# Optimization experiments

Hardware: AMD Instinct MI355X
Metric: run time of the kernel (lower is better)

## Reference

```python
import jax, jax.numpy as jnp
import numpy as np

B, L, K, D = 1024, 128, 16, 512
NUM_FEATURES, NUM_LABELS, NUM_NEG = 100000, 131072, 2048
EPS = 0.1
C = 2.0 + EPS  # spherical kernel constant


def safe_log(x, eps=1e-08):
    return jnp.log(jnp.maximum(x, eps))


def safe_normalize(x, axis=-1, eps=0.0001):
    norm = jnp.linalg.norm(x, axis=axis, keepdims=True)
    return x / jnp.maximum(norm, eps)


def setup_inputs() -> dict:
    key = jax.random.key(0)
    k0, k1, k2, k3, k4 = jax.random.split(key, 5)
    indices = jax.random.randint(k0, (B, L), 0, NUM_FEATURES)
    mask = jnp.ones((B, L), jnp.float32)
    labels = jax.random.randint(k1, (B, K), 0, NUM_LABELS)
    label_mask = jnp.ones((B, K), jnp.float32)
    neg_indices = jax.random.randint(k2, (NUM_NEG,), 0, NUM_LABELS)
    embed_table = jax.random.normal(k3, (NUM_FEATURES, D), jnp.float32) * 0.02
    W_kernel = jax.random.normal(k4, (D, NUM_LABELS), jnp.float32) * 0.02  # nnx.Linear kernel (in, out)
    return {"indices": indices, "mask": mask, "labels": labels,
            "label_mask": label_mask, "neg_indices": neg_indices,
            "embed_table": embed_table, "W_kernel": W_kernel}


def reference(indices, mask, labels, label_mask, neg_indices, embed_table, W_kernel):
    # MeanEmbedding encoder
    embeds = embed_table[indices]                                  # [B, L, D]
    sum_embeds = jnp.sum(embeds * mask[:, :, None], axis=1)        # [B, D]
    enc = sum_embeds / jnp.maximum(jnp.sum(mask, axis=1, keepdims=True), 1.0)
    query = safe_normalize(enc, axis=-1)                           # [B, D]
    W = safe_normalize(W_kernel.T, axis=-1)                        # [NUM_LABELS, D]

    safe_labels = jnp.maximum(labels, 0)
    all_indices = jnp.concatenate([safe_labels.reshape(-1), neg_indices])  # [B*K + NN]
    W_subset = W[all_indices]                                      # [B*K+NN, D]

    # spherical Yat kernel: dot^2 / max(C - 2*dot, eps)
    dot = jnp.clip(query @ W_subset.T, -0.999, 0.999)              # [B, B*K+NN]
    scores = dot ** 2 / jnp.maximum(C - 2.0 * dot, EPS)

    idx_offsets = jnp.arange(B)[:, None] * K + jnp.arange(K)[None, :]
    pos_scores = jnp.take_along_axis(scores, idx_offsets, axis=1)  # [B, K]
    neg_scores = scores[:, B * K:]                                 # [B, NN]
    all_scores = jnp.concatenate([pos_scores, neg_scores], axis=1) + 1e-08
    log_Z = jax.scipy.special.logsumexp(safe_log(all_scores), axis=1)
    log_probs = safe_log(pos_scores + 1e-08) - log_Z[:, None]
    return -jnp.sum(log_probs * label_mask) / (jnp.sum(label_mask) + 1e-06)
```

## Files before the change

kernel.cpp:

```cpp
#include <hip/hip_runtime.h>
#include <hip/hip_bf16.h>

#define BDIM 1024
#define LDIM 128
#define KDIM 16
#define DDIM 512
#define NLAB 131072
#define NNEG 2048
#define NPOS (BDIM * KDIM)
#define NSUB (NPOS + NNEG)
#define EPSV 0.1f
#define CV 2.1f
#define NBUCK 512
#define GT_BLOCKS (NBUCK * 8)

typedef __attribute__((ext_vector_type(8))) short s8v;
typedef __attribute__((ext_vector_type(4))) float f4v;
typedef __attribute__((ext_vector_type(4))) float fv4;

static __device__ __forceinline__ unsigned short f2bf(float x) {
    union { float f; unsigned u; } v; v.f = x;
    unsigned r = v.u + 0x7FFF + ((v.u >> 16) & 1);
    return (unsigned short)(r >> 16);
}
static __device__ __forceinline__ float bf2f(unsigned short h) {
    return __uint_as_float((unsigned)h << 16);
}

__global__ __launch_bounds__(256) void init_kernel(float* __restrict__ norms2,
                                                   float* __restrict__ Zrow,
                                                   float* __restrict__ accum,
                                                   int* __restrict__ ticket) {
    int j = blockIdx.x * 256 + threadIdx.x;
    if (j < NSUB) norms2[j] = 0.f;
    if (j < BDIM) Zrow[j] = 0.f;
    if (j < 2) accum[j] = 0.f;
    if (j == 0) *ticket = 0;
}

__global__ __launch_bounds__(1024) void sortall_kernel(const int* __restrict__ labels,
                                                       const int* __restrict__ negs,
                                                       int* __restrict__ offs_end,
                                                       int* __restrict__ cntg,
                                                       int* __restrict__ srt_v,
                                                       int* __restrict__ rank) {
    __shared__ int sc[NBUCK];
    int t = threadIdx.x;
    if (t < NBUCK) sc[t] = 0;
    __syncthreads();
    int vs[NSUB / 1024];
    #pragma unroll
    for (int k = 0; k < NSUB / 1024; ++k) {
        int j = k * 1024 + t;
        int v = (j < NPOS) ? max(labels[j], 0) : negs[j - NPOS];
        vs[k] = v;
        atomicAdd(&sc[v >> 8], 1);
    }
    __syncthreads();
    int c = (t < NBUCK) ? sc[t] : 0;
    for (int off = 1; off < NBUCK; off <<= 1) {
        int v2 = (t < NBUCK && t >= off) ? sc[t - off] : 0;
        __syncthreads();
        if (t < NBUCK) sc[t] += v2;
        __syncthreads();
    }
    if (t < NBUCK) { cntg[t] = c; sc[t] -= c; }
    __syncthreads();
    #pragma unroll
    for (int k = 0; k < NSUB / 1024; ++k) {
        int j = k * 1024 + t;
        int v = vs[k];
        int r = atomicAdd(&sc[v >> 8], 1);
        srt_v[r] = v;
        rank[j] = r;
    }
    __syncthreads();
    if (t < NBUCK) offs_end[t] = sc[t];
}

__global__ __launch_bounds__(256) void main1_kernel(const float* __restrict__ Wk,
                                                    const int* __restrict__ srt_v,
                                                    const int* __restrict__ offs_end,
                                                    const int* __restrict__ cnt,
                                                    unsigned short* __restrict__ WT,
                                                    float* __restrict__ norms2,
                                                    const int* __restrict__ indices,
                                                    const float* __restrict__ mask,
                                                    const float* __restrict__ embed,
                                                    float* __restrict__ query,
                                                    unsigned short* __restrict__ qbf) {
    __shared__ __align__(16) unsigned short tile[256][65];
    int t = threadIdx.x;
    int w = t >> 6, l = t & 63;

    if (blockIdx.x < BDIM) {
        char* base = (char*)&tile[0][0];
        int*   sidx    = (int*)base;
        float* smask   = (float*)(base + 512);
        float* partial = (float*)(base + 1024);
        float* red     = (float*)(base + 1024 + 8192);
        float* snorm   = (float*)(base + 1024 + 8192 + 16);
        int b = blockIdx.x;
        if (t < LDIM) {
            sidx[t]  = indices[b * LDIM + t];
            smask[t] = mask[b * LDIM + t];
        }
        __syncthreads();
        fv4 a0 = {0.f, 0.f, 0.f, 0.f}, a1 = {0.f, 0.f, 0.f, 0.f};
        #pragma unroll 4
        for (int i = 0; i < 32; ++i) {
            int row = w * 32 + i;
            int idx = sidx[row];
            float m = smask[row];
            const float* rp = &embed[(size_t)idx * DDIM + l * 8];
            fv4 v0 = *(const fv4*)rp;
            fv4 v1 = *(const fv4*)(rp + 4);
            a0 += v0 * m;
            a1 += v1 * m;
        }
        *(fv4*)&partial[w * 512 + l * 8]     = a0;
        *(fv4*)&partial[w * 512 + l * 8 + 4] = a1;
        float msum = 0.f;
        for (int i = 0; i < LDIM; ++i) msum += smask[i];
        __syncthreads();
        int c0 = t * 2;
        float x = partial[c0]       + partial[512 + c0]     + partial[1024 + c0]     + partial[1536 + c0];
        float y = partial[c0 + 1]   + partial[512 + c0 + 1] + partial[1024 + c0 + 1] + partial[1536 + c0 + 1];
        float denom = fmaxf(msum, 1.0f);
        x /= denom; y /= denom;
        float ss = x * x + y * y;
        #pragma unroll
        for (int off = 32; off > 0; off >>= 1) ss += __shfl_xor(ss, off, 64);
        __syncthreads();
        if (l == 0) red[w] = ss;
        __syncthreads();
        if (t == 0) snorm[0] = sqrtf(red[0] + red[1] + red[2] + red[3]);
        __syncthreads();
        float inv = 1.f / fmaxf(snorm[0], 1e-4f);
        x *= inv; y *= inv;
        float2 o = { x, y };
        *(float2*)&query[(size_t)b * DDIM + c0] = o;
        ushort2 ob = { f2bf(x), f2bf(y) };
        *(ushort2*)&qbf[(size_t)b * DDIM + c0] = ob;
    } else {
        int bt = blockIdx.x - BDIM;
        int g  = bt >> 3;
        int dt = bt & 7;
        int d0 = dt * 64;
        #pragma unroll
        for (int i = 0; i < 16; ++i) {
            int dl = w * 16 + i;
            fv4 v = __builtin_nontemporal_load(
                (const fv4*)&Wk[(size_t)(d0 + dl) * NLAB + g * 256 + l * 4]);
            tile[l * 4 + 0][dl] = f2bf(v[0]);
            tile[l * 4 + 1][dl] = f2bf(v[1]);
            tile[l * 4 + 2][dl] = f2bf(v[2]);
            tile[l * 4 + 3][dl] = f2bf(v[3]);
        }
        __syncthreads();
        int rend = offs_end[g];
        int rbeg = rend - cnt[g];
        for (int r = rbeg + w; r < rend; r += 4) {
            int v = srt_v[r];
            int col = v - g * 256;
            unsigned short h = tile[col][l];
            __builtin_nontemporal_store(h, &WT[(size_t)r * DDIM + d0 + l]);
            float f = bf2f(h);
            float ss = f * f;
            ss += __shfl_xor(ss, 1, 64);  ss += __shfl_xor(ss, 2, 64);
            ss += __shfl_xor(ss, 4, 64);  ss += __shfl_xor(ss, 8, 64);
            ss += __shfl_xor(ss, 16, 64); ss += __shfl_xor(ss, 32, 64);
            if (l == 0) atomicAdd(&norms2[r], ss);
        }
    }
}

static __device__ __forceinline__ float score_of(float acc, float nn) {
    float dot = acc / nn;
    dot = fminf(fmaxf(dot, -0.999f), 0.999f);
    return dot * dot / fmaxf(CV - 2.f * dot, EPSV);
}

__global__ __launch_bounds__(256) void main2_kernel(const unsigned short* __restrict__ qbf,
                                                    const float* __restrict__ query,
                                                    const unsigned short* __restrict__ WT,
                                                    const int* __restrict__ rank,
                                                    const float* __restrict__ norms2,
                                                    float* __restrict__ pos_scores,
                                                    float* __restrict__ Zrow) {
    int t = threadIdx.x;
    int w = t >> 6, l = t & 63;
    if (blockIdx.x < (BDIM / 64) * (NNEG / 64)) {
        __shared__ float rowsum[64];
        int bx = blockIdx.x;
        int mt = bx & 15, nt = bx >> 4;
        int wm = w >> 1, wn = w & 1;
        int lr = l & 15, lg = l >> 4;
        int m0 = mt * 64 + wm * 32;
        int n0 = nt * 64 + wn * 32;
        if (t < 64) rowsum[t] = 0.f;
        __syncthreads();

        int rB0 = rank[NPOS + n0 + lr];
        int rB1 = rank[NPOS + n0 + 16 + lr];
        const unsigned short* a0p = qbf + (size_t)(m0 + lr) * DDIM + lg * 8;
        const unsigned short* a1p = qbf + (size_t)(m0 + 16 + lr) * DDIM + lg * 8;
        const unsigned short* b0p = WT + (size_t)rB0 * DDIM + lg * 8;
        const unsigned short* b1p = WT + (size_t)rB1 * DDIM + lg * 8;

        f4v acc00 = {0.f, 0.f, 0.f, 0.f}, acc01 = acc00, acc10 = acc00, acc11 = acc00;
        #pragma unroll
        for (int k0 = 0; k0 < DDIM; k0 += 32) {
            s8v a0 = *(const s8v*)(a0p + k0);
            s8v a1 = *(const s8v*)(a1p + k0);
            s8v b0 = *(const s8v*)(b0p + k0);
            s8v b1 = *(const s8v*)(b1p + k0);
            acc00 = __builtin_amdgcn_mfma_f32_16x16x32_bf16(a0, b0, acc00, 0, 0, 0);
            acc01 = __builtin_amdgcn_mfma_f32_16x16x32_bf16(a0, b1, acc01, 0, 0, 0);
            acc10 = __builtin_amdgcn_mfma_f32_16x16x32_bf16(a1, b0, acc10, 0, 0, 0);
            acc11 = __builtin_amdgcn_mfma_f32_16x16x32_bf16(a1, b1, acc11, 0, 0, 0);
        }

        float nn0 = fmaxf(sqrtf(norms2[rB0]), 1e-4f);
        float nn1 = fmaxf(sqrtf(norms2[rB1]), 1e-4f);
        float s[8];
        #pragma unroll
        for (int i = 0; i < 4; ++i) {
            s[i]     = score_of(acc00[i], nn0) + score_of(acc01[i], nn1);
            s[4 + i] = score_of(acc10[i], nn0) + score_of(acc11[i], nn1);
        }
        #pragma unroll
        for (int i = 0; i < 8; ++i) {
            s[i] += __shfl_xor(s[i], 1, 64);
            s[i] += __shfl_xor(s[i], 2, 64);
            s[i] += __shfl_xor(s[i], 4, 64);
            s[i] += __shfl_xor(s[i], 8, 64);
        }
        if (lr == 0) {
            #pragma unroll
            for (int i = 0; i < 4; ++i) {
                atomicAdd(&rowsum[wm * 32 + lg * 4 + i], s[i]);
                atomicAdd(&rowsum[wm * 32 + 16 + lg * 4 + i], s[4 + i]);
            }
        }
        __syncthreads();
        if (t < 64) atomicAdd(&Zrow[mt * 64 + t], rowsum[t]);
    } else {
        int px = blockIdx.x - (BDIM / 64) * (NNEG / 64);
        int b = px * 4 + w;
        int j = b * KDIM + (l & 15);
        int r = rank[j];
        int g = l >> 4;
        const unsigned short* wrow = WT + (size_t)r * DDIM + g * 128;
        const float* qrow = query + (size_t)b * DDIM + g * 128;
        float acc = 0.f;
        #pragma unroll
        for (int kk = 0; kk < 128; kk += 8) {
            ushort4 w0 = *(const ushort4*)&wrow[kk];
            ushort4 w1 = *(const ushort4*)&wrow[kk + 4];
            float4 q0 = *(const float4*)&qrow[kk];
            float4 q1 = *(const float4*)&qrow[kk + 4];
            acc += bf2f(w0.x) * q0.x + bf2f(w0.y) * q0.y + bf2f(w0.z) * q0.z + bf2f(w0.w) * q0.w
                 + bf2f(w1.x) * q1.x + bf2f(w1.y) * q1.y + bf2f(w1.z) * q1.z + bf2f(w1.w) * q1.w;
        }
        acc += __shfl_xor(acc, 16, 64);
        acc += __shfl_xor(acc, 32, 64);
        if (l < 16) {
            float nrm = fmaxf(sqrtf(norms2[r]), 1e-4f);
            float dot = fminf(fmaxf(acc / nrm, -0.999f), 0.999f);
            float sc = dot * dot / fmaxf(CV - 2.f * dot, EPSV);
            pos_scores[j] = sc;
            float s = sc;
            s += __shfl_xor(s, 1, 64); s += __shfl_xor(s, 2, 64);
            s += __shfl_xor(s, 4, 64); s += __shfl_xor(s, 8, 64);
            if (l == 0) atomicAdd(&Zrow[b], s);
        }
    }
}

__global__ __launch_bounds__(256) void finalize_kernel(const float* __restrict__ pos_scores,
                                                       const float* __restrict__ label_mask,
                                                       const float* __restrict__ Zrow,
                                                       float* __restrict__ accum,
                                                       int* __restrict__ ticket,
                                                       float* __restrict__ out) {
    int j = blockIdx.x * 256 + threadIdx.x;
    int b = j >> 4;
    float lm = label_mask[j];
    float logZ = logf(Zrow[b] + (float)(KDIM + NNEG) * 1e-8f);
    float v = lm * (logf(pos_scores[j] + 1e-8f) - logZ);
    #pragma unroll
    for (int off = 32; off > 0; off >>= 1) {
        v  += __shfl_down(v, off, 64);
        lm += __shfl_down(lm, off, 64);
    }
    __shared__ float rv[4], rl[4];
    int wid = threadIdx.x >> 6, lane = threadIdx.x & 63;
    if (lane == 0) { rv[wid] = v; rl[wid] = lm; }
    __syncthreads();
    if (threadIdx.x == 0) {
        atomicAdd(&accum[0], rv[0] + rv[1] + rv[2] + rv[3]);
        atomicAdd(&accum[1], rl[0] + rl[1] + rl[2] + rl[3]);
        __threadfence();
        int old = atomicAdd(ticket, 1);
        if (old == (int)gridDim.x - 1) {
            float a = atomicAdd(&accum[0], 0.f);
            float m = atomicAdd(&accum[1], 0.f);
            out[0] = -a / (m + 1e-6f);
        }
    }
}

extern "C" void kernel_launch(void* const* d_in, const int* in_sizes, int n_in,
                              void* d_out, int out_size, void* d_ws, size_t ws_size,
                              hipStream_t stream) {
    const int*   indices    = (const int*)  d_in[0];
    const float* mask       = (const float*)d_in[1];
    const int*   labels     = (const int*)  d_in[2];
    const float* label_mask = (const float*)d_in[3];
    const int*   negs       = (const int*)  d_in[4];
    const float* embed      = (const float*)d_in[5];
    const float* Wk         = (const float*)d_in[6];
    float* out = (float*)d_out;

    unsigned short* WT  = (unsigned short*)d_ws;
    float* query      = (float*)(WT + (size_t)NSUB * DDIM);
    unsigned short* qbf = (unsigned short*)(query + (size_t)BDIM * DDIM);
    int*   srt_v      = (int*)(qbf + (size_t)BDIM * DDIM);
    int*   rank       = srt_v + NSUB;
    float* norms2     = (float*)(rank + NSUB);
    float* pos_scores = norms2 + NSUB;
    float* Zrow       = pos_scores + NPOS;
    float* accum      = Zrow + BDIM;
    int*   ticket     = (int*)(accum + 2);
    int*   cntg       = ticket + 1;
    int*   offs_end   = cntg + NBUCK;

    init_kernel<<<NSUB / 256, 256, 0, stream>>>(norms2, Zrow, accum, ticket);
    sortall_kernel<<<1, 1024, 0, stream>>>(labels, negs, offs_end, cntg, srt_v, rank);
    main1_kernel<<<BDIM + GT_BLOCKS, 256, 0, stream>>>(Wk, srt_v, offs_end, cntg, WT, norms2,
                                                       indices, mask, embed, query, qbf);
    main2_kernel<<<(BDIM / 64) * (NNEG / 64) + NPOS / 64, 256, 0, stream>>>(
        qbf, query, WT, rank, norms2, pos_scores, Zrow);
    finalize_kernel<<<NPOS / 256, 256, 0, stream>>>(pos_scores, label_mask, Zrow,
                                                    accum, ticket, out);
}
```

Baseline: 152.0 us.

## Merge init into sort kernel, interleave main1 blocks, drop fp32 query buffer

```diff
diff --git a/kernel.cpp b/kernel.cpp
--- a/kernel.cpp
+++ b/kernel.cpp
@@ -13,6 +13,7 @@
 #define CV 2.1f
 #define NBUCK 512
 #define GT_BLOCKS (NBUCK * 8)
+#define M1_BLOCKS (BDIM + GT_BLOCKS)
 
 typedef __attribute__((ext_vector_type(8))) short s8v;
 typedef __attribute__((ext_vector_type(4))) float f4v;
@@ -27,25 +28,26 @@
     return __uint_as_float((unsigned)h << 16);
 }
 
-__global__ __launch_bounds__(256) void init_kernel(float* __restrict__ norms2,
-                                                   float* __restrict__ Zrow,
-                                                   float* __restrict__ accum,
-                                                   int* __restrict__ ticket) {
-    int j = blockIdx.x * 256 + threadIdx.x;
-    if (j < NSUB) norms2[j] = 0.f;
-    if (j < BDIM) Zrow[j] = 0.f;
-    if (j < 2) accum[j] = 0.f;
-    if (j == 0) *ticket = 0;
-}
-
-__global__ __launch_bounds__(1024) void sortall_kernel(const int* __restrict__ labels,
-                                                       const int* __restrict__ negs,
-                                                       int* __restrict__ offs_end,
-                                                       int* __restrict__ cntg,
-                                                       int* __restrict__ srt_v,
-                                                       int* __restrict__ rank) {
+__global__ __launch_bounds__(1024) void sortinit_kernel(const int* __restrict__ labels,
+                                                        const int* __restrict__ negs,
+                                                        int* __restrict__ offs_end,
+                                                        int* __restrict__ cntg,
+                                                        int* __restrict__ srt_v,
+                                                        int* __restrict__ rank,
+                                                        float* __restrict__ norms2,
+                                                        float* __restrict__ Zrow,
+                                                        float* __restrict__ accum,
+                                                        int* __restrict__ ticket) {
+    int t = threadIdx.x;
+    if (blockIdx.x != 0) {
+        int j = (blockIdx.x - 1) * 1024 + t;
+        if (j < NSUB) norms2[j] = 0.f;
+        if (j < BDIM) Zrow[j] = 0.f;
+        if (j < 2) accum[j] = 0.f;
+        if (j == 0) *ticket = 0;
+        return;
+    }
     __shared__ int sc[NBUCK];
-    int t = threadIdx.x;
     if (t < NBUCK) sc[t] = 0;
     __syncthreads();
     int vs[NSUB / 1024];
@@ -87,20 +89,20 @@
                                                     const int* __restrict__ indices,
                                                     const float* __restrict__ mask,
                                                     const float* __restrict__ embed,
-                                                    float* __restrict__ query,
                                                     unsigned short* __restrict__ qbf) {
     __shared__ __align__(16) unsigned short tile[256][65];
     int t = threadIdx.x;
     int w = t >> 6, l = t & 63;
-
-    if (blockIdx.x < BDIM) {
+    int bx = blockIdx.x;
+
+    if (bx % 5 == 0) {
         char* base = (char*)&tile[0][0];
         int*   sidx    = (int*)base;
         float* smask   = (float*)(base + 512);
         float* partial = (float*)(base + 1024);
         float* red     = (float*)(base + 1024 + 8192);
         float* snorm   = (float*)(base + 1024 + 8192 + 16);
-        int b = blockIdx.x;
+        int b = bx / 5;
         if (t < LDIM) {
             sidx[t]  = indices[b * LDIM + t];
             smask[t] = mask[b * LDIM + t];
@@ -124,26 +126,23 @@
         for (int i = 0; i < LDIM; ++i) msum += smask[i];
         __syncthreads();
         int c0 = t * 2;
-        float x = partial[c0]       + partial[512 + c0]     + partial[1024 + c0]     + partial[1536 + c0];
-        float y = partial[c0 + 1]   + partial[512 + c0 + 1] + partial[1024 + c0 + 1] + partial[1536 + c0 + 1];
+        float x = partial[c0]     + partial[512 + c0]     + partial[1024 + c0]     + partial[1536 + c0];
+        float y = partial[c0 + 1] + partial[512 + c0 + 1] + partial[1024 + c0 + 1] + partial[1536 + c0 + 1];
         float denom = fmaxf(msum, 1.0f);
         x /= denom; y /= denom;
         float ss = x * x + y * y;
         #pragma unroll
         for (int off = 32; off > 0; off >>= 1) ss += __shfl_xor(ss, off, 64);
-        __syncthreads();
         if (l == 0) red[w] = ss;
         __syncthreads();
         if (t == 0) snorm[0] = sqrtf(red[0] + red[1] + red[2] + red[3]);
         __syncthreads();
         float inv = 1.f / fmaxf(snorm[0], 1e-4f);
         x *= inv; y *= inv;
-        float2 o = { x, y };
-        *(float2*)&query[(size_t)b * DDIM + c0] = o;
         ushort2 ob = { f2bf(x), f2bf(y) };
         *(ushort2*)&qbf[(size_t)b * DDIM + c0] = ob;
     } else {
-        int bt = blockIdx.x - BDIM;
+        int bt = bx - bx / 5 - 1;
         int g  = bt >> 3;
         int dt = bt & 7;
         int d0 = dt * 64;
@@ -182,7 +181,6 @@
 }
 
 __global__ __launch_bounds__(256) void main2_kernel(const unsigned short* __restrict__ qbf,
-                                                    const float* __restrict__ query,
                                                     const unsigned short* __restrict__ WT,
                                                     const int* __restrict__ rank,
                                                     const float* __restrict__ norms2,
@@ -252,16 +250,18 @@
         int r = rank[j];
         int g = l >> 4;
         const unsigned short* wrow = WT + (size_t)r * DDIM + g * 128;
-        const float* qrow = query + (size_t)b * DDIM + g * 128;
+        const unsigned short* qrow = qbf + (size_t)b * DDIM + g * 128;
         float acc = 0.f;
         #pragma unroll
         for (int kk = 0; kk < 128; kk += 8) {
             ushort4 w0 = *(const ushort4*)&wrow[kk];
             ushort4 w1 = *(const ushort4*)&wrow[kk + 4];
-            float4 q0 = *(const float4*)&qrow[kk];
-            float4 q1 = *(const float4*)&qrow[kk + 4];
-            acc += bf2f(w0.x) * q0.x + bf2f(w0.y) * q0.y + bf2f(w0.z) * q0.z + bf2f(w0.w) * q0.w
-                 + bf2f(w1.x) * q1.x + bf2f(w1.y) * q1.y + bf2f(w1.z) * q1.z + bf2f(w1.w) * q1.w;
+            ushort4 q0 = *(const ushort4*)&qrow[kk];
+            ushort4 q1 = *(const ushort4*)&qrow[kk + 4];
+            acc += bf2f(w0.x) * bf2f(q0.x) + bf2f(w0.y) * bf2f(q0.y)
+                 + bf2f(w0.z) * bf2f(q0.z) + bf2f(w0.w) * bf2f(q0.w)
+                 + bf2f(w1.x) * bf2f(q1.x) + bf2f(w1.y) * bf2f(q1.y)
+                 + bf2f(w1.z) * bf2f(q1.z) + bf2f(w1.w) * bf2f(q1.w);
         }
         acc += __shfl_xor(acc, 16, 64);
         acc += __shfl_xor(acc, 32, 64);
@@ -324,8 +324,7 @@
     float* out = (float*)d_out;
 
     unsigned short* WT  = (unsigned short*)d_ws;
-    float* query      = (float*)(WT + (size_t)NSUB * DDIM);
-    unsigned short* qbf = (unsigned short*)(query + (size_t)BDIM * DDIM);
+    unsigned short* qbf = WT + (size_t)NSUB * DDIM;
     int*   srt_v      = (int*)(qbf + (size_t)BDIM * DDIM);
     int*   rank       = srt_v + NSUB;
     float* norms2     = (float*)(rank + NSUB);
@@ -336,12 +335,13 @@
     int*   cntg       = ticket + 1;
     int*   offs_end   = cntg + NBUCK;
 
-    init_kernel<<<NSUB / 256, 256, 0, stream>>>(norms2, Zrow, accum, ticket);
-    sortall_kernel<<<1, 1024, 0, stream>>>(labels, negs, offs_end, cntg, srt_v, rank);
-    main1_kernel<<<BDIM + GT_BLOCKS, 256, 0, stream>>>(Wk, srt_v, offs_end, cntg, WT, norms2,
-                                                       indices, mask, embed, query, qbf);
+    sortinit_kernel<<<1 + NSUB / 1024, 1024, 0, stream>>>(labels, negs, offs_end, cntg,
+                                                          srt_v, rank, norms2, Zrow,
+                                                          accum, ticket);
+    main1_kernel<<<M1_BLOCKS, 256, 0, stream>>>(Wk, srt_v, offs_end, cntg, WT, norms2,
+                                                indices, mask, embed, qbf);
     main2_kernel<<<(BDIM / 64) * (NNEG / 64) + NPOS / 64, 256, 0, stream>>>(
-        qbf, query, WT, rank, norms2, pos_scores, Zrow);
+        qbf, WT, rank, norms2, pos_scores, Zrow);
     finalize_kernel<<<NPOS / 256, 256, 0, stream>>>(pos_scores, label_mask, Zrow,
                                                     accum, ticket, out);
 }
```

Measured after the change: 139.8 us. 8.1% less time.
